# Optimization experiments

Hardware: AMD Instinct MI355X
Metric: run time of the kernel (lower is better)

Reference implementation:

```python
import jax, jax.numpy as jnp
import numpy as np

N_NODES = 50000
N_EDGES = 800000
D = 64        # input_nf == output_nf
HID = 64      # hidden_nf
NQ = 3        # n_qubits
NORM = 100.0  # normalization_factor, aggregation_method='sum'
MU = 0.5      # hardcoded self.mu

silu = jax.nn.silu
_Zv = jnp.array([1.0, -1.0])


def _zax(q):
    # Z eigenvalues broadcast along qubit axis q of a [N,2,2,2] statevector
    return _Zv.reshape(tuple(2 if k == q else 1 for k in range(NQ)))


def _quantum_circuit(x, alpha, beta, gamma, delta, Lam):
    """Batched 3-qubit statevector simulation of the PennyLane circuit.
    x: [N, NQ] per-node rotation inputs. Returns [N, NQ] Pauli-Z expvals."""
    N = x.shape[0]
    st = jnp.zeros((N, 2, 2, 2), jnp.complex64).at[:, 0, 0, 0].set(1.0)

    def ap(st, U, q):  # apply 2x2 gate U ([2,2] const or [N,2,2] batched) on qubit q
        st = jnp.moveaxis(st, 1 + q, 3)
        sub = 'nij,nabj->nabi' if U.ndim == 3 else 'ij,nabj->nabi'
        st = jnp.einsum(sub, U, st)
        return jnp.moveaxis(st, 3, 1 + q)

    def rz(st, theta, q):  # diagonal RZ(theta) with per-node theta [N]
        ph = jnp.exp(-0.5j * theta.astype(jnp.complex64)[:, None] * _Zv)  # [N,2]
        return st * ph.reshape((N,) + tuple(2 if k == q else 1 for k in range(NQ)))

    def ry_mat(theta):  # [N] -> [N,2,2]
        c, s = jnp.cos(theta / 2), jnp.sin(theta / 2)
        return jnp.stack([jnp.stack([c, -s], -1), jnp.stack([s, c], -1)], -2).astype(jnp.complex64)

    cb, sb = jnp.cos(beta / 2), jnp.sin(beta / 2)
    RX = jnp.stack([jnp.stack([cb + 0j, -1j * sb]), jnp.stack([-1j * sb, cb + 0j])])
    Hm = jnp.array([[1.0, 1.0], [1.0, -1.0]], jnp.complex64) / np.sqrt(2.0)

    # 1) data-encoding RY layer
    for q in range(NQ):
        st = ap(st, ry_mat(x[:, q] * alpha), q)
    # 2) coupling Hamiltonian: IsingZZ(gamma*(Lam_ij+Lam_ji)/2) on each pair (diagonal phase)
    for i in range(NQ):
        for j in range(i + 1, NQ):
            phi = gamma * (Lam[i, j] + Lam[j, i]) / 2
            st = st * jnp.exp(-0.5j * phi * (_zax(i) * _zax(j)))[None]
    # 3) kinetic RX layer
    for q in range(NQ):
        st = ap(st, RX, q)
    # 4) anharmonic layer: RZ, H, RZ, H per qubit
    for q in range(NQ):
        st = rz(st, delta * (1.0 - MU * x[:, q] ** 2), q)
        st = ap(st, Hm, q)
        st = rz(st, delta * x[:, q] ** 2, q)
        st = ap(st, Hm, q)
    # 5) final kinetic RX layer
    for q in range(NQ):
        st = ap(st, RX, q)

    probs = jnp.abs(st) ** 2  # [N,2,2,2]
    return jnp.stack([jnp.sum(probs * _zax(q)[None], axis=(1, 2, 3)) for q in range(NQ)], axis=1)


def setup_inputs() -> dict:
    key = jax.random.key(0)
    ks = jax.random.split(key, 10)
    def w(k, shape):
        return jax.random.normal(k, shape, jnp.float32) * 0.05
    h = jax.random.normal(ks[0], (N_NODES, D), jnp.float32)
    edge_index = jax.random.randint(ks[1], (2, N_EDGES), 0, N_NODES)
    Lam = jnp.full((NQ, NQ), -0.1 / (NQ - 1), jnp.float32).at[jnp.arange(NQ), jnp.arange(NQ)].set(0.1)
    return {
        'h': h, 'edge_index': edge_index,
        'eW1': w(ks[2], (2 * D, HID)), 'eb1': jnp.zeros(HID, jnp.float32),
        'eW2': w(ks[3], (HID, HID)), 'eb2': jnp.zeros(HID, jnp.float32),
        'qW1': w(ks[4], (D + HID, HID)), 'qb1': jnp.zeros(HID, jnp.float32),
        'qW2': w(ks[5], (HID, NQ)), 'qb2': jnp.zeros(NQ, jnp.float32),
        'pW1': w(ks[6], (D + HID + NQ, HID)), 'pb1': jnp.zeros(HID, jnp.float32),
        'pW2': w(ks[7], (HID, D)), 'pb2': jnp.zeros(D, jnp.float32),
        'alpha': jnp.float32(0.1 / NQ), 'beta': jnp.float32(np.pi / (4 * NQ)),
        'gamma': jnp.float32(0.1 / NQ), 'delta': jnp.float32(0.05),
        'Lambda': Lam,
    }


def reference(h, edge_index, eW1, eb1, eW2, eb2, qW1, qb1, qW2, qb2,
              pW1, pb1, pW2, pb2, alpha, beta, gamma, delta, Lambda):
    row, col = edge_index[0], edge_index[1]
    # edge model (no attention, no edge_attr, no edge_mask)
    e_in = jnp.concatenate([h[row], h[col]], axis=1)           # [E, 2D]
    mij = silu(silu(e_in @ eW1 + eb1) @ eW2 + eb2)             # [E, HID]
    # node model: scatter-sum aggregation normalized by factor ('sum' mode)
    agg = jax.ops.segment_sum(mij, row, num_segments=N_NODES) / NORM
    a = jnp.concatenate([h, agg], axis=1)                      # [N, D+HID]
    q_in = silu(a @ qW1 + qb1) @ qW2 + qb2                     # [N, NQ]
    # original detaches inputs and rebuilds outputs via torch.tensor -> no grad flow
    q_out = jax.lax.stop_gradient(
        _quantum_circuit(jax.lax.stop_gradient(q_in), alpha, beta, gamma, delta, Lambda)
    ).astype(h.dtype)
    a2 = jnp.concatenate([a, q_out], axis=1)                   # [N, 2*HID+NQ]
    out = h + (silu(a2 @ pW1 + pb1) @ pW2 + pb2)
    return out, mij
```

## Files before the change

kernel.cpp:

```cpp
#include <hip/hip_runtime.h>
#include <hip/hip_bf16.h>
#include <math.h>


#define N_NODES 50000
#define N_EDGES 800000
#define DIM 64
#define HID 64

typedef __bf16 bf16_t;
typedef __bf16 bf16x8 __attribute__((ext_vector_type(8)));
typedef float f32x4 __attribute__((ext_vector_type(4)));

__device__ __forceinline__ float silu_f(float x) {
    return x / (1.f + __expf(-x));
}

__device__ __forceinline__ f32x4 mfma16(bf16x8 a, bf16x8 b, f32x4 c) {
    return __builtin_amdgcn_mfma_f32_16x16x32_bf16(a, b, c, 0, 0, 0);
}

__device__ __forceinline__ bf16x8 cvt8(const float* __restrict__ p) {
    f32x4 u0 = *(const f32x4*)p;
    f32x4 u1 = *(const f32x4*)(p + 4);
    bf16x8 r;
    r[0] = (bf16_t)u0[0]; r[1] = (bf16_t)u0[1]; r[2] = (bf16_t)u0[2]; r[3] = (bf16_t)u0[3];
    r[4] = (bf16_t)u1[0]; r[5] = (bf16_t)u1[1]; r[6] = (bf16_t)u1[2]; r[7] = (bf16_t)u1[3];
    return r;
}

__global__ __launch_bounds__(256) void zero_kernel(float* __restrict__ p, int n4)
{
    int i = blockIdx.x * 256 + threadIdx.x;
    if (i < n4) {
        f32x4 z = {0.f, 0.f, 0.f, 0.f};
        *(f32x4*)(p + (size_t)i * 4) = z;
    }
}

__global__ __launch_bounds__(256) void edge_kernel(
    const float* __restrict__ h,
    const int* __restrict__ ei,
    const float* __restrict__ eW1, const float* __restrict__ eb1,
    const float* __restrict__ eW2, const float* __restrict__ eb2,
    float* __restrict__ mij_out,
    float* __restrict__ agg)
{
    __shared__ __align__(16) bf16_t sB1[64][136];
    __shared__ __align__(16) bf16_t sB2[64][72];
    __shared__ __align__(16) bf16_t sHid[4][16][72];
    __shared__ float sb1[64], sb2[64];

    const int tid = threadIdx.x;
    for (int idx = tid; idx < 128 * 64; idx += 256) {
        int k = idx >> 6, n = idx & 63;
        sB1[n][k] = (bf16_t)eW1[idx];
    }
    for (int idx = tid; idx < 64 * 64; idx += 256) {
        int k = idx >> 6, n = idx & 63;
        sB2[n][k] = (bf16_t)eW2[idx];
    }
    if (tid < 64) { sb1[tid] = eb1[tid]; sb2[tid] = eb2[tid]; }
    __syncthreads();

    const int lane = tid & 63, wave = tid >> 6;
    const int m = lane & 15, quad = lane >> 4;
    const int e0 = (blockIdx.x * 4 + wave) * 16;
    const int e = e0 + m;
    const int nrow = ei[e];
    const int ncol = ei[N_EDGES + e];
    const float* ra = h + (size_t)nrow * DIM;
    const float* rb = h + (size_t)ncol * DIM;

    const f32x4 z = {0.f, 0.f, 0.f, 0.f};
    f32x4 acc[4] = {z, z, z, z};
    #pragma unroll
    for (int ks = 0; ks < 4; ++ks) {
        const int k0 = ks * 32 + quad * 8;
        const float* src = (k0 < 64) ? (ra + k0) : (rb + (k0 - 64));
        bf16x8 a = cvt8(src);
        #pragma unroll
        for (int nt = 0; nt < 4; ++nt) {
            bf16x8 b = *(const bf16x8*)&sB1[nt * 16 + m][k0];
            acc[nt] = mfma16(a, b, acc[nt]);
        }
    }

    #pragma unroll
    for (int nt = 0; nt < 4; ++nt) {
        #pragma unroll
        for (int rr = 0; rr < 4; ++rr) {
            int row = quad * 4 + rr;
            int col = nt * 16 + m;
            sHid[wave][row][col] = (bf16_t)silu_f(acc[nt][rr] + sb1[col]);
        }
    }
    __syncthreads();

    f32x4 acc2[4] = {z, z, z, z};
    #pragma unroll
    for (int ks = 0; ks < 2; ++ks) {
        const int k0 = ks * 32 + quad * 8;
        bf16x8 a = *(const bf16x8*)&sHid[wave][m][k0];
        #pragma unroll
        for (int nt = 0; nt < 4; ++nt) {
            bf16x8 b = *(const bf16x8*)&sB2[nt * 16 + m][k0];
            acc2[nt] = mfma16(a, b, acc2[nt]);
        }
    }

    #pragma unroll
    for (int nt = 0; nt < 4; ++nt) {
        #pragma unroll
        for (int rr = 0; rr < 4; ++rr) {
            int row = quad * 4 + rr;
            int col = nt * 16 + m;
            float v = silu_f(acc2[nt][rr] + sb2[col]);
            int ee = e0 + row;
            mij_out[(size_t)ee * HID + col] = v;
            int dst = __shfl(nrow, row);
            unsafeAtomicAdd(&agg[dst * HID + col], v);
        }
    }
}

__global__ __launch_bounds__(256) void node_kernel(
    const float* __restrict__ h, const float* __restrict__ agg,
    const float* __restrict__ qW1, const float* __restrict__ qb1,
    const float* __restrict__ qW2, const float* __restrict__ qb2,
    const float* __restrict__ pW1, const float* __restrict__ pb1,
    const float* __restrict__ pW2, const float* __restrict__ pb2,
    const float* __restrict__ al_p, const float* __restrict__ be_p,
    const float* __restrict__ ga_p, const float* __restrict__ de_p,
    const float* __restrict__ lam_p,
    float* __restrict__ out)
{
    __shared__ __align__(16) bf16_t sQ1[64][136];
    __shared__ __align__(16) bf16_t sP1[64][168];
    __shared__ __align__(16) bf16_t sP2[64][72];
    __shared__ __align__(16) bf16_t sHid[4][16][72];
    __shared__ float sQ2[192];
    __shared__ float sqb1[64], spb1[64], spb2[64], sqb2[3];
    __shared__ float sQout[4][16][3];

    const int tid = threadIdx.x;
    for (int idx = tid; idx < 128 * 64; idx += 256) { int k = idx >> 6, n = idx & 63; sQ1[n][k] = (bf16_t)qW1[idx]; }
    for (int idx = tid; idx < 131 * 64; idx += 256) { int k = idx >> 6, n = idx & 63; sP1[n][k] = (bf16_t)pW1[idx]; }
    for (int idx = tid; idx < 29 * 64; idx += 256) { int k = 131 + (idx >> 6), n = idx & 63; sP1[n][k] = (bf16_t)0.f; }
    for (int idx = tid; idx < 64 * 64; idx += 256) { int k = idx >> 6, n = idx & 63; sP2[n][k] = (bf16_t)pW2[idx]; }
    if (tid < 192) sQ2[tid] = qW2[tid];
    if (tid < 64) { sqb1[tid] = qb1[tid]; spb1[tid] = pb1[tid]; spb2[tid] = pb2[tid]; }
    if (tid < 3) sqb2[tid] = qb2[tid];
    __syncthreads();

    const int lane = tid & 63, wave = tid >> 6;
    const int m = lane & 15, quad = lane >> 4;
    const int n0 = (blockIdx.x * 4 + wave) * 16;
    const int nm = min(n0 + m, N_NODES - 1);
    const float* hrow = h + (size_t)nm * DIM;
    const float* grow = agg + (size_t)nm * HID;

    const f32x4 z = {0.f, 0.f, 0.f, 0.f};

    f32x4 acc[4] = {z, z, z, z};
    #pragma unroll
    for (int ks = 0; ks < 4; ++ks) {
        const int k0 = ks * 32 + quad * 8;
        bf16x8 a;
        if (k0 < 64) {
            a = cvt8(hrow + k0);
        } else {
            const float* g = grow + (k0 - 64);
            f32x4 u0 = *(const f32x4*)g;
            f32x4 u1 = *(const f32x4*)(g + 4);
            #pragma unroll
            for (int j = 0; j < 4; ++j) { a[j] = (bf16_t)(u0[j] * 0.01f); a[4 + j] = (bf16_t)(u1[j] * 0.01f); }
        }
        #pragma unroll
        for (int nt = 0; nt < 4; ++nt) {
            bf16x8 b = *(const bf16x8*)&sQ1[nt * 16 + m][k0];
            acc[nt] = mfma16(a, b, acc[nt]);
        }
    }
    #pragma unroll
    for (int nt = 0; nt < 4; ++nt) {
        #pragma unroll
        for (int rr = 0; rr < 4; ++rr) {
            int row = quad * 4 + rr, col = nt * 16 + m;
            sHid[wave][row][col] = (bf16_t)silu_f(acc[nt][rr] + sqb1[col]);
        }
    }
    __syncthreads();

    const float al = al_p[0], be = be_p[0];
    const float ga = ga_p[0], de = de_p[0];

    if (lane < 16) {
        float qin[3];
        #pragma unroll
        for (int c = 0; c < 3; ++c) {
            float s = sqb2[c];
            for (int k = 0; k < 64; ++k)
                s += (float)sHid[wave][lane][k] * sQ2[k * 3 + c];
            qin[c] = s;
        }
        float re[8], im[8];
        float cc[3], ssn[3];
        #pragma unroll
        for (int q = 0; q < 3; ++q) {
            float th = 0.5f * qin[q] * al;
            cc[q] = cosf(th); ssn[q] = sinf(th);
        }
        #pragma unroll
        for (int i = 0; i < 8; ++i) {
            float v0 = (i & 4) ? ssn[0] : cc[0];
            float v1 = (i & 2) ? ssn[1] : cc[1];
            float v2 = (i & 1) ? ssn[2] : cc[2];
            re[i] = v0 * v1 * v2; im[i] = 0.f;
        }
        float phi01 = ga * (lam_p[1] + lam_p[3]) * 0.5f;
        float phi02 = ga * (lam_p[2] + lam_p[6]) * 0.5f;
        float phi12 = ga * (lam_p[5] + lam_p[7]) * 0.5f;
        #pragma unroll
        for (int i = 0; i < 8; ++i) {
            float z0 = (i & 4) ? -1.f : 1.f;
            float z1 = (i & 2) ? -1.f : 1.f;
            float z2 = (i & 1) ? -1.f : 1.f;
            float th = -0.5f * (phi01 * z0 * z1 + phi02 * z0 * z2 + phi12 * z1 * z2);
            float ct = cosf(th), st = sinf(th);
            float r = re[i], iM = im[i];
            re[i] = r * ct - iM * st;
            im[i] = r * st + iM * ct;
        }
        float cb = cosf(0.5f * be), sb = sinf(0.5f * be);
        auto rx = [&](int q) {
            int msk = 4 >> q;
            #pragma unroll
            for (int i = 0; i < 8; ++i) {
                if (i & msk) continue;
                int j = i | msk;
                float r0 = re[i], i0 = im[i], r1 = re[j], i1 = im[j];
                re[i] = cb * r0 + sb * i1;
                im[i] = cb * i0 - sb * r1;
                re[j] = sb * i0 + cb * r1;
                im[j] = -sb * r0 + cb * i1;
            }
        };
        auto hgate = [&](int q) {
            const float inv = 0.70710678f;
            int msk = 4 >> q;
            #pragma unroll
            for (int i = 0; i < 8; ++i) {
                if (i & msk) continue;
                int j = i | msk;
                float r0 = re[i], i0 = im[i], r1 = re[j], i1 = im[j];
                re[i] = (r0 + r1) * inv; im[i] = (i0 + i1) * inv;
                re[j] = (r0 - r1) * inv; im[j] = (i0 - i1) * inv;
            }
        };
        auto rzg = [&](int q, float th) {
            int msk = 4 >> q;
            float c = cosf(0.5f * th), s = sinf(0.5f * th);
            #pragma unroll
            for (int i = 0; i < 8; ++i) {
                float sg = (i & msk) ? s : -s;
                float r = re[i], iM = im[i];
                re[i] = r * c - iM * sg;
                im[i] = r * sg + iM * c;
            }
        };
        rx(0); rx(1); rx(2);
        #pragma unroll
        for (int q = 0; q < 3; ++q) {
            float x = qin[q];
            rzg(q, de * (1.f - 0.5f * x * x));
            hgate(q);
            rzg(q, de * x * x);
            hgate(q);
        }
        rx(0); rx(1); rx(2);
        float e0v = 0.f, e1v = 0.f, e2v = 0.f;
        #pragma unroll
        for (int i = 0; i < 8; ++i) {
            float p = re[i] * re[i] + im[i] * im[i];
            e0v += (i & 4) ? -p : p;
            e1v += (i & 2) ? -p : p;
            e2v += (i & 1) ? -p : p;
        }
        sQout[wave][lane][0] = e0v;
        sQout[wave][lane][1] = e1v;
        sQout[wave][lane][2] = e2v;
    }
    __syncthreads();

    f32x4 acc2[4] = {z, z, z, z};
    #pragma unroll
    for (int ks = 0; ks < 5; ++ks) {
        const int k0 = ks * 32 + quad * 8;
        bf16x8 a;
        if (k0 < 64) {
            a = cvt8(hrow + k0);
        } else if (k0 < 128) {
            const float* g = grow + (k0 - 64);
            f32x4 u0 = *(const f32x4*)g;
            f32x4 u1 = *(const f32x4*)(g + 4);
            #pragma unroll
            for (int j = 0; j < 4; ++j) { a[j] = (bf16_t)(u0[j] * 0.01f); a[4 + j] = (bf16_t)(u1[j] * 0.01f); }
        } else {
            #pragma unroll
            for (int j = 0; j < 8; ++j) a[j] = (bf16_t)0.f;
            if (k0 == 128) {
                a[0] = (bf16_t)sQout[wave][m][0];
                a[1] = (bf16_t)sQout[wave][m][1];
                a[2] = (bf16_t)sQout[wave][m][2];
            }
        }
        #pragma unroll
        for (int nt = 0; nt < 4; ++nt) {
            bf16x8 b = *(const bf16x8*)&sP1[nt * 16 + m][k0];
            acc2[nt] = mfma16(a, b, acc2[nt]);
        }
    }
    #pragma unroll
    for (int nt = 0; nt < 4; ++nt) {
        #pragma unroll
        for (int rr = 0; rr < 4; ++rr) {
            int row = quad * 4 + rr, col = nt * 16 + m;
            sHid[wave][row][col] = (bf16_t)silu_f(acc2[nt][rr] + spb1[col]);
        }
    }
    __syncthreads();

    f32x4 acc3[4] = {z, z, z, z};
    #pragma unroll
    for (int ks = 0; ks < 2; ++ks) {
        const int k0 = ks * 32 + quad * 8;
        bf16x8 a = *(const bf16x8*)&sHid[wave][m][k0];
        #pragma unroll
        for (int nt = 0; nt < 4; ++nt) {
            bf16x8 b = *(const bf16x8*)&sP2[nt * 16 + m][k0];
            acc3[nt] = mfma16(a, b, acc3[nt]);
        }
    }
    #pragma unroll
    for (int nt = 0; nt < 4; ++nt) {
        #pragma unroll
        for (int rr = 0; rr < 4; ++rr) {
            int row = quad * 4 + rr, col = nt * 16 + m;
            int node = n0 + row;
            if (node < N_NODES) {
                float v = acc3[nt][rr] + spb2[col] + h[(size_t)node * DIM + col];
                out[(size_t)node * DIM + col] = v;
            }
        }
    }
}

extern "C" void kernel_launch(void* const* d_in, const int* in_sizes, int n_in,
                              void* d_out, int out_size, void* d_ws, size_t ws_size,
                              hipStream_t stream)
{
    const float* h   = (const float*)d_in[0];
    const int* ei    = (const int*)d_in[1];
    const float* eW1 = (const float*)d_in[2];
    const float* eb1 = (const float*)d_in[3];
    const float* eW2 = (const float*)d_in[4];
    const float* eb2 = (const float*)d_in[5];
    const float* qW1 = (const float*)d_in[6];
    const float* qb1 = (const float*)d_in[7];
    const float* qW2 = (const float*)d_in[8];
    const float* qb2 = (const float*)d_in[9];
    const float* pW1 = (const float*)d_in[10];
    const float* pb1 = (const float*)d_in[11];
    const float* pW2 = (const float*)d_in[12];
    const float* pb2 = (const float*)d_in[13];
    const float* al  = (const float*)d_in[14];
    const float* be  = (const float*)d_in[15];
    const float* ga  = (const float*)d_in[16];
    const float* de  = (const float*)d_in[17];
    const float* lam = (const float*)d_in[18];

    float* out = (float*)d_out;
    float* mij = out + (size_t)N_NODES * DIM;
    float* agg = (float*)d_ws;

    const int n4 = (N_NODES * HID) / 4;
    zero_kernel<<<(n4 + 255) / 256, 256, 0, stream>>>(agg, n4);
    edge_kernel<<<N_EDGES / 64, 256, 0, stream>>>(h, ei, eW1, eb1, eW2, eb2, mij, agg);
    node_kernel<<<(N_NODES + 63) / 64, 256, 0, stream>>>(h, agg, qW1, qb1, qW2, qb2,
                                                         pW1, pb1, pW2, pb2,
                                                         al, be, ga, de, lam, out);
}
```

Baseline: 451.0 us.

## Use bf16 node features and packed bf16 atomics with persistent edge/node kernels

Adds a pre-pass that converts h to bf16, staged in the output buffer, so edge gathers read half the bytes. Aggregation moves to a bf16 buffer updated with packed global_atomic_pk_add_bf16, halving atomic traffic, and the 1/100 scale is folded into the weights. Both kernels become persistent grid-stride loops with 512-thread blocks, and redundant __syncthreads are dropped. The node kernel's qW2 projection now runs on MFMA, and outputs use nontemporal stores. Accumulating the sum in bf16 costs precision.

```diff
diff --git a/kernel.cpp b/kernel.cpp
--- a/kernel.cpp
+++ b/kernel.cpp
@@ -1,12 +1,17 @@
 #include <hip/hip_runtime.h>
 #include <hip/hip_bf16.h>
 #include <math.h>
+#include <stdint.h>
 
 
 #define N_NODES 50000
 #define N_EDGES 800000
 #define DIM 64
 #define HID 64
+#define T_EDGE (N_EDGES / 16)
+#define T_NODE (N_NODES / 16)
+#define EDGE_GRID 768
+#define NODE_GRID 512
 
 typedef __bf16 bf16_t;
 typedef __bf16 bf16x8 __attribute__((ext_vector_type(8)));
@@ -29,6 +34,13 @@
     return r;
 }
 
+__device__ __forceinline__ void atomic_pk_bf16(bf16_t* p, float lo, float hi) {
+    union { bf16_t h2[2]; uint32_t u; } pk;
+    pk.h2[0] = (bf16_t)lo; pk.h2[1] = (bf16_t)hi;
+    asm volatile("global_atomic_pk_add_bf16 %0, %1, off"
+                 :: "v"((uint64_t)(uintptr_t)p), "v"(pk.u) : "memory");
+}
+
 __global__ __launch_bounds__(256) void zero_kernel(float* __restrict__ p, int n4)
 {
     int i = blockIdx.x * 256 + threadIdx.x;
@@ -38,25 +50,34 @@
     }
 }
 
-__global__ __launch_bounds__(256) void edge_kernel(
-    const float* __restrict__ h,
+__global__ __launch_bounds__(256) void cvt_kernel(const float* __restrict__ h,
+                                                  bf16_t* __restrict__ hb, int n8)
+{
+    int i = blockIdx.x * 256 + threadIdx.x;
+    if (i < n8) {
+        *(bf16x8*)(hb + (size_t)i * 8) = cvt8(h + (size_t)i * 8);
+    }
+}
+
+__global__ __launch_bounds__(512, 6) void edge_kernel(
+    const bf16_t* __restrict__ hb,
     const int* __restrict__ ei,
     const float* __restrict__ eW1, const float* __restrict__ eb1,
     const float* __restrict__ eW2, const float* __restrict__ eb2,
     float* __restrict__ mij_out,
-    float* __restrict__ agg)
+    bf16_t* __restrict__ agg)
 {
     __shared__ __align__(16) bf16_t sB1[64][136];
     __shared__ __align__(16) bf16_t sB2[64][72];
-    __shared__ __align__(16) bf16_t sHid[4][16][72];
+    __shared__ __align__(16) bf16_t sHid[8][16][72];
     __shared__ float sb1[64], sb2[64];
 
     const int tid = threadIdx.x;
-    for (int idx = tid; idx < 128 * 64; idx += 256) {
+    for (int idx = tid; idx < 128 * 64; idx += 512) {
         int k = idx >> 6, n = idx & 63;
         sB1[n][k] = (bf16_t)eW1[idx];
     }
-    for (int idx = tid; idx < 64 * 64; idx += 256) {
+    for (int idx = tid; idx < 64 * 64; idx += 512) {
         int k = idx >> 6, n = idx & 63;
         sB2[n][k] = (bf16_t)eW2[idx];
     }
@@ -65,67 +86,74 @@
 
     const int lane = tid & 63, wave = tid >> 6;
     const int m = lane & 15, quad = lane >> 4;
-    const int e0 = (blockIdx.x * 4 + wave) * 16;
-    const int e = e0 + m;
-    const int nrow = ei[e];
-    const int ncol = ei[N_EDGES + e];
-    const float* ra = h + (size_t)nrow * DIM;
-    const float* rb = h + (size_t)ncol * DIM;
-
     const f32x4 z = {0.f, 0.f, 0.f, 0.f};
-    f32x4 acc[4] = {z, z, z, z};
-    #pragma unroll
-    for (int ks = 0; ks < 4; ++ks) {
-        const int k0 = ks * 32 + quad * 8;
-        const float* src = (k0 < 64) ? (ra + k0) : (rb + (k0 - 64));
-        bf16x8 a = cvt8(src);
+
+    for (int t = blockIdx.x * 8 + wave; t < T_EDGE; t += EDGE_GRID * 8) {
+        const int e0 = t * 16;
+        const int e = e0 + m;
+        const int nrow = ei[e];
+        const int ncol = ei[N_EDGES + e];
+        const bf16_t* ra = hb + (size_t)nrow * DIM;
+        const bf16_t* rb = hb + (size_t)ncol * DIM;
+
+        f32x4 acc[4] = {z, z, z, z};
+        #pragma unroll
+        for (int ks = 0; ks < 4; ++ks) {
+            const int k0 = ks * 32 + quad * 8;
+            const bf16_t* src = (k0 < 64) ? (ra + k0) : (rb + (k0 - 64));
+            bf16x8 a = *(const bf16x8*)src;
+            #pragma unroll
+            for (int nt = 0; nt < 4; ++nt) {
+                bf16x8 b = *(const bf16x8*)&sB1[nt * 16 + m][k0];
+                acc[nt] = mfma16(a, b, acc[nt]);
+            }
+        }
+
         #pragma unroll
         for (int nt = 0; nt < 4; ++nt) {
-            bf16x8 b = *(const bf16x8*)&sB1[nt * 16 + m][k0];
-            acc[nt] = mfma16(a, b, acc[nt]);
-        }
-    }
-
-    #pragma unroll
-    for (int nt = 0; nt < 4; ++nt) {
-        #pragma unroll
-        for (int rr = 0; rr < 4; ++rr) {
-            int row = quad * 4 + rr;
-            int col = nt * 16 + m;
-            sHid[wave][row][col] = (bf16_t)silu_f(acc[nt][rr] + sb1[col]);
-        }
-    }
-    __syncthreads();
-
-    f32x4 acc2[4] = {z, z, z, z};
-    #pragma unroll
-    for (int ks = 0; ks < 2; ++ks) {
-        const int k0 = ks * 32 + quad * 8;
-        bf16x8 a = *(const bf16x8*)&sHid[wave][m][k0];
+            #pragma unroll
+            for (int rr = 0; rr < 4; ++rr) {
+                int row = quad * 4 + rr;
+                int col = nt * 16 + m;
+                sHid[wave][row][col] = (bf16_t)silu_f(acc[nt][rr] + sb1[col]);
+            }
+        }
+
+        f32x4 acc2[4] = {z, z, z, z};
+        #pragma unroll
+        for (int ks = 0; ks < 2; ++ks) {
+            const int k0 = ks * 32 + quad * 8;
+            bf16x8 a = *(const bf16x8*)&sHid[wave][m][k0];
+            #pragma unroll
+            for (int nt = 0; nt < 4; ++nt) {
+                bf16x8 b = *(const bf16x8*)&sB2[nt * 16 + m][k0];
+                acc2[nt] = mfma16(a, b, acc2[nt]);
+            }
+        }
+
+        int dstrow[4];
+        #pragma unroll
+        for (int rr = 0; rr < 4; ++rr) dstrow[rr] = __shfl(nrow, quad * 4 + rr);
+
         #pragma unroll
         for (int nt = 0; nt < 4; ++nt) {
-            bf16x8 b = *(const bf16x8*)&sB2[nt * 16 + m][k0];
-            acc2[nt] = mfma16(a, b, acc2[nt]);
-        }
-    }
-
-    #pragma unroll
-    for (int nt = 0; nt < 4; ++nt) {
-        #pragma unroll
-        for (int rr = 0; rr < 4; ++rr) {
-            int row = quad * 4 + rr;
-            int col = nt * 16 + m;
-            float v = silu_f(acc2[nt][rr] + sb2[col]);
-            int ee = e0 + row;
-            mij_out[(size_t)ee * HID + col] = v;
-            int dst = __shfl(nrow, row);
-            unsafeAtomicAdd(&agg[dst * HID + col], v);
-        }
-    }
-}
-
-__global__ __launch_bounds__(256) void node_kernel(
-    const float* __restrict__ h, const float* __restrict__ agg,
+            #pragma unroll
+            for (int rr = 0; rr < 4; ++rr) {
+                int row = quad * 4 + rr;
+                int col = nt * 16 + m;
+                float v = silu_f(acc2[nt][rr] + sb2[col]);
+                __builtin_nontemporal_store(v, &mij_out[(size_t)(e0 + row) * HID + col]);
+                float vh = __shfl_xor(v, 1);
+                if ((lane & 1) == 0) {
+                    atomic_pk_bf16(agg + (size_t)dstrow[rr] * HID + col, v, vh);
+                }
+            }
+        }
+    }
+}
+
+__global__ __launch_bounds__(512, 4) void node_kernel(
+    const float* __restrict__ h, const bf16_t* __restrict__ aggb,
     const float* __restrict__ qW1, const float* __restrict__ qb1,
     const float* __restrict__ qW2, const float* __restrict__ qb2,
     const float* __restrict__ pW1, const float* __restrict__ pb1,
@@ -138,219 +166,229 @@
     __shared__ __align__(16) bf16_t sQ1[64][136];
     __shared__ __align__(16) bf16_t sP1[64][168];
     __shared__ __align__(16) bf16_t sP2[64][72];
-    __shared__ __align__(16) bf16_t sHid[4][16][72];
-    __shared__ float sQ2[192];
-    __shared__ float sqb1[64], spb1[64], spb2[64], sqb2[3];
-    __shared__ float sQout[4][16][3];
+    __shared__ __align__(16) bf16_t sQ2b[16][72];
+    __shared__ __align__(16) bf16_t sHid[8][16][72];
+    __shared__ float sQio[8][16][4];
+    __shared__ float sqb1[64], spb1[64], spb2[64], sqb2[4];
 
     const int tid = threadIdx.x;
-    for (int idx = tid; idx < 128 * 64; idx += 256) { int k = idx >> 6, n = idx & 63; sQ1[n][k] = (bf16_t)qW1[idx]; }
-    for (int idx = tid; idx < 131 * 64; idx += 256) { int k = idx >> 6, n = idx & 63; sP1[n][k] = (bf16_t)pW1[idx]; }
-    for (int idx = tid; idx < 29 * 64; idx += 256) { int k = 131 + (idx >> 6), n = idx & 63; sP1[n][k] = (bf16_t)0.f; }
-    for (int idx = tid; idx < 64 * 64; idx += 256) { int k = idx >> 6, n = idx & 63; sP2[n][k] = (bf16_t)pW2[idx]; }
-    if (tid < 192) sQ2[tid] = qW2[tid];
+    for (int idx = tid; idx < 128 * 64; idx += 512) {
+        int k = idx >> 6, n = idx & 63;
+        float w = qW1[idx];
+        sQ1[n][k] = (bf16_t)(k < 64 ? w : w * 0.01f);
+    }
+    for (int idx = tid; idx < 131 * 64; idx += 512) {
+        int k = idx >> 6, n = idx & 63;
+        float w = pW1[idx];
+        sP1[n][k] = (bf16_t)((k >= 64 && k < 128) ? w * 0.01f : w);
+    }
+    for (int idx = tid; idx < 37 * 64; idx += 512) {
+        int k = 131 + (idx >> 6), n = idx & 63;
+        sP1[n][k] = (bf16_t)0.f;
+    }
+    for (int idx = tid; idx < 64 * 64; idx += 512) {
+        int k = idx >> 6, n = idx & 63;
+        sP2[n][k] = (bf16_t)pW2[idx];
+    }
+    for (int idx = tid; idx < 16 * 72; idx += 512) {
+        int c = idx / 72, k = idx - c * 72;
+        sQ2b[c][k] = (bf16_t)((c < 3 && k < 64) ? qW2[k * 3 + c] : 0.f);
+    }
     if (tid < 64) { sqb1[tid] = qb1[tid]; spb1[tid] = pb1[tid]; spb2[tid] = pb2[tid]; }
     if (tid < 3) sqb2[tid] = qb2[tid];
     __syncthreads();
 
     const int lane = tid & 63, wave = tid >> 6;
     const int m = lane & 15, quad = lane >> 4;
-    const int n0 = (blockIdx.x * 4 + wave) * 16;
-    const int nm = min(n0 + m, N_NODES - 1);
-    const float* hrow = h + (size_t)nm * DIM;
-    const float* grow = agg + (size_t)nm * HID;
-
-    const f32x4 z = {0.f, 0.f, 0.f, 0.f};
-
-    f32x4 acc[4] = {z, z, z, z};
-    #pragma unroll
-    for (int ks = 0; ks < 4; ++ks) {
-        const int k0 = ks * 32 + quad * 8;
-        bf16x8 a;
-        if (k0 < 64) {
-            a = cvt8(hrow + k0);
-        } else {
-            const float* g = grow + (k0 - 64);
-            f32x4 u0 = *(const f32x4*)g;
-            f32x4 u1 = *(const f32x4*)(g + 4);
-            #pragma unroll
-            for (int j = 0; j < 4; ++j) { a[j] = (bf16_t)(u0[j] * 0.01f); a[4 + j] = (bf16_t)(u1[j] * 0.01f); }
-        }
-        #pragma unroll
-        for (int nt = 0; nt < 4; ++nt) {
-            bf16x8 b = *(const bf16x8*)&sQ1[nt * 16 + m][k0];
-            acc[nt] = mfma16(a, b, acc[nt]);
-        }
-    }
-    #pragma unroll
-    for (int nt = 0; nt < 4; ++nt) {
-        #pragma unroll
-        for (int rr = 0; rr < 4; ++rr) {
-            int row = quad * 4 + rr, col = nt * 16 + m;
-            sHid[wave][row][col] = (bf16_t)silu_f(acc[nt][rr] + sqb1[col]);
-        }
-    }
-    __syncthreads();
-
     const float al = al_p[0], be = be_p[0];
     const float ga = ga_p[0], de = de_p[0];
-
-    if (lane < 16) {
-        float qin[3];
-        #pragma unroll
-        for (int c = 0; c < 3; ++c) {
-            float s = sqb2[c];
-            for (int k = 0; k < 64; ++k)
-                s += (float)sHid[wave][lane][k] * sQ2[k * 3 + c];
-            qin[c] = s;
-        }
-        float re[8], im[8];
-        float cc[3], ssn[3];
-        #pragma unroll
-        for (int q = 0; q < 3; ++q) {
-            float th = 0.5f * qin[q] * al;
-            cc[q] = cosf(th); ssn[q] = sinf(th);
-        }
-        #pragma unroll
-        for (int i = 0; i < 8; ++i) {
-            float v0 = (i & 4) ? ssn[0] : cc[0];
-            float v1 = (i & 2) ? ssn[1] : cc[1];
-            float v2 = (i & 1) ? ssn[2] : cc[2];
-            re[i] = v0 * v1 * v2; im[i] = 0.f;
-        }
-        float phi01 = ga * (lam_p[1] + lam_p[3]) * 0.5f;
-        float phi02 = ga * (lam_p[2] + lam_p[6]) * 0.5f;
-        float phi12 = ga * (lam_p[5] + lam_p[7]) * 0.5f;
-        #pragma unroll
-        for (int i = 0; i < 8; ++i) {
-            float z0 = (i & 4) ? -1.f : 1.f;
-            float z1 = (i & 2) ? -1.f : 1.f;
-            float z2 = (i & 1) ? -1.f : 1.f;
-            float th = -0.5f * (phi01 * z0 * z1 + phi02 * z0 * z2 + phi12 * z1 * z2);
-            float ct = cosf(th), st = sinf(th);
-            float r = re[i], iM = im[i];
-            re[i] = r * ct - iM * st;
-            im[i] = r * st + iM * ct;
-        }
-        float cb = cosf(0.5f * be), sb = sinf(0.5f * be);
-        auto rx = [&](int q) {
-            int msk = 4 >> q;
+    const float phi01 = ga * (lam_p[1] + lam_p[3]) * 0.5f;
+    const float phi02 = ga * (lam_p[2] + lam_p[6]) * 0.5f;
+    const float phi12 = ga * (lam_p[5] + lam_p[7]) * 0.5f;
+    const float cbg = cosf(0.5f * be), sbg = sinf(0.5f * be);
+    const f32x4 z = {0.f, 0.f, 0.f, 0.f};
+
+    for (int t = blockIdx.x * 8 + wave; t < T_NODE; t += NODE_GRID * 8) {
+        const int n0 = t * 16;
+        const float* hrow = h + (size_t)(n0 + m) * DIM;
+        const bf16_t* grow = aggb + (size_t)(n0 + m) * HID;
+
+        f32x4 acc[4] = {z, z, z, z};
+        #pragma unroll
+        for (int ks = 0; ks < 4; ++ks) {
+            const int k0 = ks * 32 + quad * 8;
+            bf16x8 a = (k0 < 64) ? cvt8(hrow + k0)
+                                 : *(const bf16x8*)(grow + (k0 - 64));
+            #pragma unroll
+            for (int nt = 0; nt < 4; ++nt) {
+                bf16x8 b = *(const bf16x8*)&sQ1[nt * 16 + m][k0];
+                acc[nt] = mfma16(a, b, acc[nt]);
+            }
+        }
+        #pragma unroll
+        for (int nt = 0; nt < 4; ++nt) {
+            #pragma unroll
+            for (int rr = 0; rr < 4; ++rr) {
+                int row = quad * 4 + rr, col = nt * 16 + m;
+                sHid[wave][row][col] = (bf16_t)silu_f(acc[nt][rr] + sqb1[col]);
+            }
+        }
+
+        f32x4 aq = z;
+        #pragma unroll
+        for (int ks = 0; ks < 2; ++ks) {
+            const int k0 = ks * 32 + quad * 8;
+            bf16x8 a = *(const bf16x8*)&sHid[wave][m][k0];
+            bf16x8 b = *(const bf16x8*)&sQ2b[m][k0];
+            aq = mfma16(a, b, aq);
+        }
+        if (m < 3) {
+            #pragma unroll
+            for (int rr = 0; rr < 4; ++rr)
+                sQio[wave][quad * 4 + rr][m] = aq[rr] + sqb2[m];
+        }
+
+        if (lane < 16) {
+            float qin[3];
+            qin[0] = sQio[wave][lane][0];
+            qin[1] = sQio[wave][lane][1];
+            qin[2] = sQio[wave][lane][2];
+            float re[8], im[8];
+            float cc[3], ssn[3];
+            #pragma unroll
+            for (int q = 0; q < 3; ++q) {
+                float th = 0.5f * qin[q] * al;
+                cc[q] = cosf(th); ssn[q] = sinf(th);
+            }
             #pragma unroll
             for (int i = 0; i < 8; ++i) {
-                if (i & msk) continue;
-                int j = i | msk;
-                float r0 = re[i], i0 = im[i], r1 = re[j], i1 = im[j];
-                re[i] = cb * r0 + sb * i1;
-                im[i] = cb * i0 - sb * r1;
-                re[j] = sb * i0 + cb * r1;
-                im[j] = -sb * r0 + cb * i1;
-            }
-        };
-        auto hgate = [&](int q) {
-            const float inv = 0.70710678f;
-            int msk = 4 >> q;
+                float v0 = (i & 4) ? ssn[0] : cc[0];
+                float v1 = (i & 2) ? ssn[1] : cc[1];
+                float v2 = (i & 1) ? ssn[2] : cc[2];
+                re[i] = v0 * v1 * v2; im[i] = 0.f;
+            }
             #pragma unroll
             for (int i = 0; i < 8; ++i) {
-                if (i & msk) continue;
-                int j = i | msk;
-                float r0 = re[i], i0 = im[i], r1 = re[j], i1 = im[j];
-                re[i] = (r0 + r1) * inv; im[i] = (i0 + i1) * inv;
-                re[j] = (r0 - r1) * inv; im[j] = (i0 - i1) * inv;
-            }
-        };
-        auto rzg = [&](int q, float th) {
-            int msk = 4 >> q;
-            float c = cosf(0.5f * th), s = sinf(0.5f * th);
+                float z0 = (i & 4) ? -1.f : 1.f;
+                float z1 = (i & 2) ? -1.f : 1.f;
+                float z2 = (i & 1) ? -1.f : 1.f;
+                float th = -0.5f * (phi01 * z0 * z1 + phi02 * z0 * z2 + phi12 * z1 * z2);
+                float ct = cosf(th), st = sinf(th);
+                float r = re[i], iM = im[i];
+                re[i] = r * ct - iM * st;
+                im[i] = r * st + iM * ct;
+            }
+            auto rx = [&](int q) {
+                int msk = 4 >> q;
+                #pragma unroll
+                for (int i = 0; i < 8; ++i) {
+                    if (i & msk) continue;
+                    int j = i | msk;
+                    float r0 = re[i], i0 = im[i], r1 = re[j], i1 = im[j];
+                    re[i] = cbg * r0 + sbg * i1;
+                    im[i] = cbg * i0 - sbg * r1;
+                    re[j] = sbg * i0 + cbg * r1;
+                    im[j] = -sbg * r0 + cbg * i1;
+                }
+            };
+            auto hgate = [&](int q) {
+                const float inv = 0.70710678f;
+                int msk = 4 >> q;
+                #pragma unroll
+                for (int i = 0; i < 8; ++i) {
+                    if (i & msk) continue;
+                    int j = i | msk;
+                    float r0 = re[i], i0 = im[i], r1 = re[j], i1 = im[j];
+                    re[i] = (r0 + r1) * inv; im[i] = (i0 + i1) * inv;
+                    re[j] = (r0 - r1) * inv; im[j] = (i0 - i1) * inv;
+                }
+            };
+            auto rzg = [&](int q, float th) {
+                int msk = 4 >> q;
+                float c = cosf(0.5f * th), s = sinf(0.5f * th);
+                #pragma unroll
+                for (int i = 0; i < 8; ++i) {
+                    float sg = (i & msk) ? s : -s;
+                    float r = re[i], iM = im[i];
+                    re[i] = r * c - iM * sg;
+                    im[i] = r * sg + iM * c;
+                }
+            };
+            rx(0); rx(1); rx(2);
+            #pragma unroll
+            for (int q = 0; q < 3; ++q) {
+                float x = qin[q];
+                rzg(q, de * (1.f - 0.5f * x * x));
+                hgate(q);
+                rzg(q, de * x * x);
+                hgate(q);
+            }
+            rx(0); rx(1); rx(2);
+            float e0v = 0.f, e1v = 0.f, e2v = 0.f;
             #pragma unroll
             for (int i = 0; i < 8; ++i) {
-                float sg = (i & msk) ? s : -s;
-                float r = re[i], iM = im[i];
-                re[i] = r * c - iM * sg;
-                im[i] = r * sg + iM * c;
-            }
-        };
-        rx(0); rx(1); rx(2);
-        #pragma unroll
-        for (int q = 0; q < 3; ++q) {
-            float x = qin[q];
-            rzg(q, de * (1.f - 0.5f * x * x));
-            hgate(q);
-            rzg(q, de * x * x);
-            hgate(q);
-        }
-        rx(0); rx(1); rx(2);
-        float e0v = 0.f, e1v = 0.f, e2v = 0.f;
-        #pragma unroll
-        for (int i = 0; i < 8; ++i) {
-            float p = re[i] * re[i] + im[i] * im[i];
-            e0v += (i & 4) ? -p : p;
-            e1v += (i & 2) ? -p : p;
-            e2v += (i & 1) ? -p : p;
-        }
-        sQout[wave][lane][0] = e0v;
-        sQout[wave][lane][1] = e1v;
-        sQout[wave][lane][2] = e2v;
-    }
-    __syncthreads();
-
-    f32x4 acc2[4] = {z, z, z, z};
-    #pragma unroll
-    for (int ks = 0; ks < 5; ++ks) {
-        const int k0 = ks * 32 + quad * 8;
-        bf16x8 a;
-        if (k0 < 64) {
-            a = cvt8(hrow + k0);
-        } else if (k0 < 128) {
-            const float* g = grow + (k0 - 64);
-            f32x4 u0 = *(const f32x4*)g;
-            f32x4 u1 = *(const f32x4*)(g + 4);
-            #pragma unroll
-            for (int j = 0; j < 4; ++j) { a[j] = (bf16_t)(u0[j] * 0.01f); a[4 + j] = (bf16_t)(u1[j] * 0.01f); }
-        } else {
-            #pragma unroll
-            for (int j = 0; j < 8; ++j) a[j] = (bf16_t)0.f;
-            if (k0 == 128) {
-                a[0] = (bf16_t)sQout[wave][m][0];
-                a[1] = (bf16_t)sQout[wave][m][1];
-                a[2] = (bf16_t)sQout[wave][m][2];
+                float p = re[i] * re[i] + im[i] * im[i];
+                e0v += (i & 4) ? -p : p;
+                e1v += (i & 2) ? -p : p;
+                e2v += (i & 1) ? -p : p;
+            }
+            sQio[wave][lane][0] = e0v;
+            sQio[wave][lane][1] = e1v;
+            sQio[wave][lane][2] = e2v;
+        }
+
+        f32x4 acc2[4] = {z, z, z, z};
+        #pragma unroll
+        for (int ks = 0; ks < 5; ++ks) {
+            const int k0 = ks * 32 + quad * 8;
+            bf16x8 a;
+            if (k0 < 64) {
+                a = cvt8(hrow + k0);
+            } else if (k0 < 128) {
+                a = *(const bf16x8*)(grow + (k0 - 64));
+            } else {
+                #pragma unroll
+                for (int j = 0; j < 8; ++j) a[j] = (bf16_t)0.f;
+                if (k0 == 128) {
+                    a[0] = (bf16_t)sQio[wave][m][0];
+                    a[1] = (bf16_t)sQio[wave][m][1];
+                    a[2] = (bf16_t)sQio[wave][m][2];
+                }
+            }
+            #pragma unroll
+            for (int nt = 0; nt < 4; ++nt) {
+                bf16x8 b = *(const bf16x8*)&sP1[nt * 16 + m][k0];
+                acc2[nt] = mfma16(a, b, acc2[nt]);
             }
         }
         #pragma unroll
         for (int nt = 0; nt < 4; ++nt) {
-            bf16x8 b = *(const bf16x8*)&sP1[nt * 16 + m][k0];
-            acc2[nt] = mfma16(a, b, acc2[nt]);
-        }
-    }
-    #pragma unroll
-    for (int nt = 0; nt < 4; ++nt) {
-        #pragma unroll
-        for (int rr = 0; rr < 4; ++rr) {
-            int row = quad * 4 + rr, col = nt * 16 + m;
-            sHid[wave][row][col] = (bf16_t)silu_f(acc2[nt][rr] + spb1[col]);
-        }
-    }
-    __syncthreads();
-
-    f32x4 acc3[4] = {z, z, z, z};
-    #pragma unroll
-    for (int ks = 0; ks < 2; ++ks) {
-        const int k0 = ks * 32 + quad * 8;
-        bf16x8 a = *(const bf16x8*)&sHid[wave][m][k0];
+            #pragma unroll
+            for (int rr = 0; rr < 4; ++rr) {
+                int row = quad * 4 + rr, col = nt * 16 + m;
+                sHid[wave][row][col] = (bf16_t)silu_f(acc2[nt][rr] + spb1[col]);
+            }
+        }
+
+        f32x4 acc3[4] = {z, z, z, z};
+        #pragma unroll
+        for (int ks = 0; ks < 2; ++ks) {
+            const int k0 = ks * 32 + quad * 8;
+            bf16x8 a = *(const bf16x8*)&sHid[wave][m][k0];
+            #pragma unroll
+            for (int nt = 0; nt < 4; ++nt) {
+                bf16x8 b = *(const bf16x8*)&sP2[nt * 16 + m][k0];
+                acc3[nt] = mfma16(a, b, acc3[nt]);
+            }
+        }
         #pragma unroll
         for (int nt = 0; nt < 4; ++nt) {
-            bf16x8 b = *(const bf16x8*)&sP2[nt * 16 + m][k0];
-            acc3[nt] = mfma16(a, b, acc3[nt]);
-        }
-    }
-    #pragma unroll
-    for (int nt = 0; nt < 4; ++nt) {
-        #pragma unroll
-        for (int rr = 0; rr < 4; ++rr) {
-            int row = quad * 4 + rr, col = nt * 16 + m;
-            int node = n0 + row;
-            if (node < N_NODES) {
+            #pragma unroll
+            for (int rr = 0; rr < 4; ++rr) {
+                int row = quad * 4 + rr, col = nt * 16 + m;
+                int node = n0 + row;
                 float v = acc3[nt][rr] + spb2[col] + h[(size_t)node * DIM + col];
-                out[(size_t)node * DIM + col] = v;
+                __builtin_nontemporal_store(v, &out[(size_t)node * DIM + col]);
             }
         }
     }
@@ -382,12 +420,16 @@
 
     float* out = (float*)d_out;
     float* mij = out + (size_t)N_NODES * DIM;
-    float* agg = (float*)d_ws;
-
-    const int n4 = (N_NODES * HID) / 4;
-    zero_kernel<<<(n4 + 255) / 256, 256, 0, stream>>>(agg, n4);
-    edge_kernel<<<N_EDGES / 64, 256, 0, stream>>>(h, ei, eW1, eb1, eW2, eb2, mij, agg);
-    node_kernel<<<(N_NODES + 63) / 64, 256, 0, stream>>>(h, agg, qW1, qb1, qW2, qb2,
-                                                         pW1, pb1, pW2, pb2,
-                                                         al, be, ga, de, lam, out);
-}
+    bf16_t* hb = (bf16_t*)d_out;
+    bf16_t* aggb = (bf16_t*)d_ws;
+
+    const int nz4 = (N_NODES * HID * (int)sizeof(bf16_t)) / 16;
+    const int n8  = (N_NODES * DIM) / 8;
+
+    zero_kernel<<<(nz4 + 255) / 256, 256, 0, stream>>>((float*)aggb, nz4);
+    cvt_kernel<<<(n8 + 255) / 256, 256, 0, stream>>>(h, hb, n8);
+    edge_kernel<<<EDGE_GRID, 512, 0, stream>>>(hb, ei, eW1, eb1, eW2, eb2, mij, aggb);
+    node_kernel<<<NODE_GRID, 512, 0, stream>>>(h, aggb, qW1, qb1, qW2, qb2,
+                                               pW1, pb1, pW2, pb2,
+                                               al, be, ga, de, lam, out);
+}
```

New measurement: 490.5 us. 1.09x slower.
